# Optimization experiments

Hardware: AMD Instinct MI355X
Metric: run time of the kernel (lower is better)

Reference implementation:

```python
import jax, jax.numpy as jnp
import numpy as np

N = 100000; E = 3200000; B = 4096
F = 128; H = 128; T1 = 574; T2 = 152; MH = 128
BN_INV = float(1.0 / np.sqrt(1.0 + 1e-5))  # eval-mode BatchNorm1d, running_mean=0, running_var=1


def setup_inputs() -> dict:
    key = jax.random.key(0)
    ks = jax.random.split(key, 16)
    def w(k, shape):
        return (jax.random.normal(k, shape, jnp.float32) / np.sqrt(shape[0])).astype(jnp.float32)
    return {
        "feats": jax.random.normal(ks[0], (N, F), jnp.float32),
        "src": jax.random.randint(ks[1], (E,), 0, N, dtype=jnp.int32),
        "dst": jax.random.randint(ks[2], (E,), 0, N, dtype=jnp.int32),
        "graph_ids": jnp.sort(jax.random.randint(ks[3], (N,), 0, B, dtype=jnp.int32)),
        "W1": w(ks[4], (F, H)), "b1": jnp.zeros((H,), jnp.float32),
        "resW1": w(ks[5], (F, H)), "resb1": jnp.zeros((H,), jnp.float32),
        "W2": w(ks[6], (H, H)), "b2": jnp.zeros((H,), jnp.float32),
        "resW2": w(ks[7], (H, H)), "resb2": jnp.zeros((H,), jnp.float32),
        "aw_W": w(ks[8], (H, 1)), "aw_b": jnp.zeros((1,), jnp.float32),
        "orW1": w(ks[9], (2 * H, MH)), "orb1": jnp.zeros((MH,), jnp.float32),
        "org": jnp.ones((MH,), jnp.float32), "orbeta": jnp.zeros((MH,), jnp.float32),
        "orW2": w(ks[10], (MH, T1)), "orb2": jnp.zeros((T1,), jnp.float32),
        "scW1": w(ks[11], (2 * H + T1, MH)), "scb1": jnp.zeros((MH,), jnp.float32),
        "scg": jnp.ones((MH,), jnp.float32), "scbeta": jnp.zeros((MH,), jnp.float32),
        "scW2": w(ks[12], (MH, T2)), "scb2": jnp.zeros((T2,), jnp.float32),
    }


def _gcn_layer(feats, src, dst, W, b, resW, resb, out_norm, in_norm):
    # GraphConv with norm='both': D_out^{-1/2} on source, sum over edges, D_in^{-1/2} on dest.
    h = (feats * out_norm[:, None]) @ W                       # [N, H]
    agg = jax.ops.segment_sum(h[src], dst, num_segments=N)    # gather-compute-scatter
    out = jax.nn.relu(agg * in_norm[:, None] + b)             # activation inside GraphConv
    return out + jax.nn.relu(feats @ resW + resb)             # dgllife residual branch


def _mlp(x, Wa, ba, gam, bet, Wb, bb):
    # dgllife MLPPredictor: Dropout(0) -> Linear -> ReLU -> BatchNorm1d(eval) -> Linear
    z = jax.nn.relu(x @ Wa + ba)
    z = gam * (z * BN_INV) + bet
    return z @ Wb + bb


def _forward(feats, src, dst, graph_ids, W1, b1, resW1, resb1, W2, b2, resW2, resb2,
             aw_W, aw_b, orW1, orb1, org, orbeta, orW2, orb2,
             scW1, scb1, scg, scbeta, scW2, scb2):
    ones = jnp.ones((E,), jnp.float32)
    out_norm = jnp.clip(jax.ops.segment_sum(ones, src, num_segments=N), 1.0) ** -0.5
    in_norm = jnp.clip(jax.ops.segment_sum(ones, dst, num_segments=N), 1.0) ** -0.5
    h = _gcn_layer(feats, src, dst, W1, b1, resW1, resb1, out_norm, in_norm)
    h = _gcn_layer(h, src, dst, W2, b2, resW2, resb2, out_norm, in_norm)
    # WeightedSumAndMax readout
    aw = jax.nn.sigmoid(h @ aw_W + aw_b)                      # [N, 1] atom weights
    hsum = jax.ops.segment_sum(aw * h, graph_ids, num_segments=B)
    hmax = jax.ops.segment_max(h, graph_ids, num_segments=B)
    hmax = jnp.where(jnp.isfinite(hmax), hmax, 0.0)           # guard empty graphs
    g = jnp.concatenate([hsum, hmax], axis=1)                 # [B, 2H]
    or_logits = _mlp(g, orW1, orb1, org, orbeta, orW2, orb2)  # [B, T1]
    scent = _mlp(jnp.concatenate([g, or_logits], axis=1), scW1, scb1, scg, scbeta, scW2, scb2)
    return or_logits, scent


def reference(feats, src, dst, graph_ids, W1, b1, resW1, resb1, W2, b2, resW2, resb2,
              aw_W, aw_b, orW1, orb1, org, orbeta, orW2, orb2,
              scW1, scb1, scg, scbeta, scW2, scb2):
    return _forward(feats, src, dst, graph_ids, W1, b1, resW1, resb1, W2, b2, resW2, resb2,
                    aw_W, aw_b, orW1, orb1, org, orbeta, orW2, orb2,
                    scW1, scb1, scg, scbeta, scW2, scb2)
```

## Files before the change

kernel.cpp:

```cpp
#include <hip/hip_runtime.h>

#define NN 100000
#define EE 3200000
#define NGRAPH 4096
#define BN_INV_F 0.99999500003749981f
#define PAD 80
#define SHIFT 8
#define NBUCK 391
#define CHUNK 8192
#define NBLK 391
#define SCAN_N (2 * NBUCK * NBLK)
#define SCHUNK 2048
#define SBLKS ((SCAN_N + SCHUNK - 1) / SCHUNK)

typedef __attribute__((ext_vector_type(8))) short short8v;
typedef __attribute__((ext_vector_type(4))) float f32x4;

__device__ inline ushort f2bf(float f) {
  uint u = __builtin_bit_cast(uint, f);
  u += 0x7fff + ((u >> 16) & 1);
  return (ushort)(u >> 16);
}
__device__ inline float bf_lo(uint v) { return __builtin_bit_cast(float, v << 16); }
__device__ inline float bf_hi(uint v) { return __builtin_bit_cast(float, v & 0xffff0000u); }

__global__ __launch_bounds__(256) void count_ab(const int* __restrict__ src,
                                                const int* __restrict__ dst,
                                                int* __restrict__ cnt) {
  __shared__ int hd[NBUCK], hs[NBUCK];
  int t = threadIdx.x, blk = blockIdx.x;
  for (int i = t; i < NBUCK; i += 256) { hd[i] = 0; hs[i] = 0; }
  __syncthreads();
  int base = blk * CHUNK;
#pragma unroll 4
  for (int j = 0; j < 32; j++) {
    int e = base + j * 256 + t;
    if (e < EE) {
      atomicAdd(&hd[((unsigned)dst[e]) >> SHIFT], 1);
      atomicAdd(&hs[((unsigned)src[e]) >> SHIFT], 1);
    }
  }
  __syncthreads();
  for (int i = t; i < NBUCK; i += 256) {
    cnt[i * NBLK + blk] = hd[i];
    cnt[(NBUCK + i) * NBLK + blk] = hs[i];
  }
}

__global__ __launch_bounds__(256) void scan1(const int* __restrict__ cnt,
                                             int* __restrict__ partial) {
  __shared__ int red[256];
  int b = blockIdx.x, t = threadIdx.x;
  int s = 0;
  for (int j = 0; j < 8; j++) { int i = b * SCHUNK + j * 256 + t; if (i < SCAN_N) s += cnt[i]; }
  red[t] = s;
  __syncthreads();
  for (int off = 128; off > 0; off >>= 1) {
    if (t < off) red[t] += red[t + off];
    __syncthreads();
  }
  if (t == 0) partial[b] = red[0];
}

__global__ void scan2(int* __restrict__ partial) {
  if (threadIdx.x == 0) {
    int run = 0;
    for (int i = 0; i < SBLKS; i++) { int v = partial[i]; partial[i] = run; run += v; }
  }
}

__global__ __launch_bounds__(256) void scan3(int* __restrict__ cnt,
                                             const int* __restrict__ partial) {
  __shared__ int wsum[4];
  int b = blockIdx.x, t = threadIdx.x;
  int lane = t & 63, wid = t >> 6;
  int base = b * SCHUNK + t * 8;
  int v[8];
#pragma unroll
  for (int j = 0; j < 8; j++) { int i = base + j; v[j] = (i < SCAN_N) ? cnt[i] : 0; }
  int s = ((v[0] + v[1]) + (v[2] + v[3])) + ((v[4] + v[5]) + (v[6] + v[7]));
  int inc = s;
#pragma unroll
  for (int off = 1; off < 64; off <<= 1) {
    int u = __shfl_up(inc, off);
    if (lane >= off) inc += u;
  }
  if (lane == 63) wsum[wid] = inc;
  __syncthreads();
  int woff = 0;
  for (int w = 0; w < wid; w++) woff += wsum[w];
  int excl = partial[b] + woff + (inc - s);
#pragma unroll
  for (int j = 0; j < 8; j++) {
    int i = base + j;
    if (i < SCAN_N) cnt[i] = excl;
    excl += v[j];
  }
}

__global__ __launch_bounds__(256) void scatter_c(const int* __restrict__ src,
                                                 const int* __restrict__ dst,
                                                 const int* __restrict__ off,
                                                 int2* __restrict__ ebuf,
                                                 int* __restrict__ sbuf) {
  __shared__ int cd[NBUCK], cs[NBUCK];
  int t = threadIdx.x, blk = blockIdx.x;
  for (int i = t; i < NBUCK; i += 256) {
    cd[i] = off[i * NBLK + blk];
    cs[i] = off[(NBUCK + i) * NBLK + blk] - EE;
  }
  __syncthreads();
  int base = blk * CHUNK;
#pragma unroll 4
  for (int j = 0; j < 32; j++) {
    int e = base + j * 256 + t;
    if (e < EE) {
      int d = dst[e], s = src[e];
      int p = atomicAdd(&cd[((unsigned)d) >> SHIFT], 1);
      ebuf[p] = make_int2(d, s);
      int q = atomicAdd(&cs[((unsigned)s) >> SHIFT], 1);
      sbuf[q] = s;
    }
  }
}

__global__ __launch_bounds__(256) void pass_dd(const int* __restrict__ off,
                                               const int2* __restrict__ ebuf,
                                               const int* __restrict__ sbuf,
                                               int* __restrict__ csrp,
                                               int* __restrict__ icnt,
                                               float* __restrict__ inrm,
                                               float* __restrict__ onrm) {
  __shared__ int cur[256], cur2[256];
  int t = threadIdx.x, b = blockIdx.x;
  cur[t] = 0; cur2[t] = 0;
  __syncthreads();
  int node0 = b << SHIFT;
  int start = off[b * NBLK];
  int end = (b == NBUCK - 1) ? EE : off[(b + 1) * NBLK];
  for (int e = start + t; e < end; e += 256) {
    int2 p = ebuf[e];
    int pos = atomicAdd(&cur[p.x - node0], 1);
    if (pos < PAD) csrp[(size_t)p.x * PAD + pos] = p.y;
  }
  int s2 = off[(NBUCK + b) * NBLK] - EE;
  int e2 = (b == NBUCK - 1) ? EE : off[(NBUCK + b + 1) * NBLK] - EE;
  for (int e = s2 + t; e < e2; e += 256)
    atomicAdd(&cur2[sbuf[e] - node0], 1);
  __syncthreads();
  int node = node0 + t;
  if (node < NN) {
    int c = cur[t];
    icnt[node] = c;
    inrm[node] = rsqrtf(fmaxf((float)c, 1.f));
    onrm[node] = rsqrtf(fmaxf((float)cur2[t], 1.f));
  }
}

__global__ __launch_bounds__(256) void conv_all(
    const float* __restrict__ W1, const float* __restrict__ rW1,
    const float* __restrict__ W2, const float* __restrict__ rW2,
    const float* __restrict__ oW1, const float* __restrict__ oW2,
    const float* __restrict__ sW1, const float* __restrict__ sW2,
    ushort* __restrict__ Wt1, ushort* __restrict__ Wr1,
    ushort* __restrict__ Wt2, ushort* __restrict__ Wr2,
    ushort* __restrict__ Wm1, ushort* __restrict__ Wm2,
    ushort* __restrict__ Wm3, ushort* __restrict__ Wm4)
{
  int b = blockIdx.x;
  const float* W; ushort* O; int K, N, Kpad, c;
  if (b < 512) {
    int which = b >> 7; c = b & 127;
    K = 128; N = 128; Kpad = 128;
    W = which == 0 ? W1 : which == 1 ? rW1 : which == 2 ? W2 : rW2;
    O = which == 0 ? Wt1 : which == 1 ? Wr1 : which == 2 ? Wt2 : Wr2;
  } else if (b < 640)  { c = b - 512;  W = oW1; O = Wm1; K = 256; N = 128; Kpad = 256; }
  else if (b < 1216)   { c = b - 640;  W = oW2; O = Wm2; K = 128; N = 574; Kpad = 128; }
  else if (b < 1344)   { c = b - 1216; W = sW1; O = Wm3; K = 830; N = 128; Kpad = 832; }
  else                 { c = b - 1344; W = sW2; O = Wm4; K = 128; N = 152; Kpad = 128; }
  for (int k = threadIdx.x; k < Kpad; k += 256)
    O[(size_t)c * Kpad + k] = (c < N && k < K) ? f2bf(W[(size_t)k * N + c]) : (ushort)0;
}

__global__ __launch_bounds__(256) void conv_x(const float* __restrict__ X,
                                              ushort* __restrict__ Xb) {
  int i = blockIdx.x * 256 + threadIdx.x;
  float4 v = *(const float4*)&X[(size_t)i * 4];
  ushort o[4] = {f2bf(v.x), f2bf(v.y), f2bf(v.z), f2bf(v.w)};
  *(ushort4*)&Xb[(size_t)i * 4] = *(ushort4*)o;
}

template<int MODE>
__global__ __launch_bounds__(256) void fused_layer(
    const ushort* __restrict__ Xg, const float* __restrict__ gscale,
    const int* __restrict__ csrp, const int* __restrict__ icnt,
    const ushort* __restrict__ Xr,
    const ushort* __restrict__ Wt, const ushort* __restrict__ Wr,
    const float* __restrict__ innorm,
    const float* __restrict__ bias, const float* __restrict__ resb,
    ushort* __restrict__ outb, float* __restrict__ outf,
    const float* __restrict__ awW, const float* __restrict__ awb,
    float* __restrict__ aw)
{
  __shared__ uint agg[64 * 68];
  int t = threadIdx.x;
  int lane = t & 63, wid = t >> 6;
  int r0 = blockIdx.x * 64;
  const uint* T32 = (const uint*)Xg;

  for (int nn = 0; nn < 16; nn++) {
    int node = r0 + wid * 16 + nn;
    float a0 = 0.f, a1 = 0.f, b0 = 0.f, b1 = 0.f;
    float c0 = 0.f, c1 = 0.f, d0 = 0.f, d1 = 0.f;
    float e0 = 0.f, e1 = 0.f, f0 = 0.f, f1 = 0.f;
    float g0 = 0.f, g1 = 0.f, h0 = 0.f, h1 = 0.f;
    if (node < NN) {
      int cnt = icnt[node]; if (cnt > PAD) cnt = PAD;
      const int* row = csrp + (size_t)node * PAD;
      int j = 0;
      for (; j + 7 < cnt; j += 8) {
        int r0i = row[j],     r1i = row[j + 1], r2i = row[j + 2], r3i = row[j + 3];
        int r4i = row[j + 4], r5i = row[j + 5], r6i = row[j + 6], r7i = row[j + 7];
        float w0 = gscale[r0i], w1 = gscale[r1i], w2 = gscale[r2i], w3 = gscale[r3i];
        float w4 = gscale[r4i], w5 = gscale[r5i], w6 = gscale[r6i], w7 = gscale[r7i];
        uint v0 = T32[(size_t)r0i * 64 + lane];
        uint v1 = T32[(size_t)r1i * 64 + lane];
        uint v2 = T32[(size_t)r2i * 64 + lane];
        uint v3 = T32[(size_t)r3i * 64 + lane];
        uint v4 = T32[(size_t)r4i * 64 + lane];
        uint v5 = T32[(size_t)r5i * 64 + lane];
        uint v6 = T32[(size_t)r6i * 64 + lane];
        uint v7 = T32[(size_t)r7i * 64 + lane];
        a0 = fmaf(w0, bf_lo(v0), a0); a1 = fmaf(w0, bf_hi(v0), a1);
        b0 = fmaf(w1, bf_lo(v1), b0); b1 = fmaf(w1, bf_hi(v1), b1);
        c0 = fmaf(w2, bf_lo(v2), c0); c1 = fmaf(w2, bf_hi(v2), c1);
        d0 = fmaf(w3, bf_lo(v3), d0); d1 = fmaf(w3, bf_hi(v3), d1);
        e0 = fmaf(w4, bf_lo(v4), e0); e1 = fmaf(w4, bf_hi(v4), e1);
        f0 = fmaf(w5, bf_lo(v5), f0); f1 = fmaf(w5, bf_hi(v5), f1);
        g0 = fmaf(w6, bf_lo(v6), g0); g1 = fmaf(w6, bf_hi(v6), g1);
        h0 = fmaf(w7, bf_lo(v7), h0); h1 = fmaf(w7, bf_hi(v7), h1);
      }
      for (; j < cnt; j++) {
        int ri = row[j];
        float w = gscale[ri];
        uint v = T32[(size_t)ri * 64 + lane];
        a0 = fmaf(w, bf_lo(v), a0); a1 = fmaf(w, bf_hi(v), a1);
      }
    }
    float s0 = ((a0 + b0) + (c0 + d0)) + ((e0 + f0) + (g0 + h0));
    float s1 = ((a1 + b1) + (c1 + d1)) + ((e1 + f1) + (g1 + h1));
    agg[(wid * 16 + nn) * 68 + lane] = (uint)f2bf(s0) | ((uint)f2bf(s1) << 16);
  }
  __syncthreads();

  int cl = lane & 15, kh = lane >> 4;
  short8v a1v[4], a2v[4];
  const uint* arow = agg + (size_t)(wid * 16 + cl) * 68;
#pragma unroll
  for (int kk = 0; kk < 4; kk++)
    a1v[kk] = *(const short8v*)(arow + kk * 16 + kh * 4);
  int xrow = r0 + wid * 16 + cl; if (xrow > NN - 1) xrow = NN - 1;
#pragma unroll
  for (int kk = 0; kk < 4; kk++)
    a2v[kk] = *(const short8v*)(Xr + (size_t)xrow * 128 + kk * 32 + kh * 8);

  f32x4 acc1[8], acc2[8];
#pragma unroll
  for (int i = 0; i < 8; i++) { acc1[i] = (f32x4){0.f,0.f,0.f,0.f}; acc2[i] = acc1[i]; }
#pragma unroll
  for (int ct = 0; ct < 8; ct++) {
#pragma unroll
    for (int kk = 0; kk < 4; kk++) {
      short8v bt = *(const short8v*)(Wt + (size_t)(ct * 16 + cl) * 128 + kk * 32 + kh * 8);
      short8v br = *(const short8v*)(Wr + (size_t)(ct * 16 + cl) * 128 + kk * 32 + kh * 8);
      acc1[ct] = __builtin_amdgcn_mfma_f32_16x16x32_bf16(a1v[kk], bt, acc1[ct], 0, 0, 0);
      acc2[ct] = __builtin_amdgcn_mfma_f32_16x16x32_bf16(a2v[kk], br, acc2[ct], 0, 0, 0);
    }
  }

#pragma unroll
  for (int r = 0; r < 4; r++) {
    int row = r0 + wid * 16 + kh * 4 + r;
    if (row >= NN) continue;
    float inr = innorm[row];
    float pr = 0.f;
#pragma unroll
    for (int ct = 0; ct < 8; ct++) {
      int col = ct * 16 + cl;
      float g  = acc1[ct][r] * inr + bias[col];
      float rs = acc2[ct][r] + resb[col];
      float v = fmaxf(g, 0.f) + fmaxf(rs, 0.f);
      if (MODE == 1) outb[(size_t)row * 128 + col] = f2bf(v);
      else { outf[(size_t)row * 128 + col] = v; pr += v * awW[col]; }
    }
    if (MODE == 2) {
#pragma unroll
      for (int off = 1; off < 16; off <<= 1) pr += __shfl_xor(pr, off);
      if (cl == 0) aw[row] = 1.f / (1.f + expf(-(pr + awb[0])));
    }
  }
}

__global__ void readout_kernel(const float* __restrict__ h,
                               const float* __restrict__ aw,
                               const int* __restrict__ gid,
                               ushort* __restrict__ xc)
{
  int gg = blockIdx.x;
  int c  = threadIdx.x;
  int lo = 0, hi = NN;
  while (lo < hi) { int mid = (lo + hi) >> 1; if (gid[mid] < gg) lo = mid + 1; else hi = mid; }
  int start = lo;
  hi = NN;
  while (lo < hi) { int mid = (lo + hi) >> 1; if (gid[mid] < gg + 1) lo = mid + 1; else hi = mid; }
  int end = lo;
  float s = 0.f, m = 0.f;
  for (int n = start; n < end; n++) {
    float v = h[(size_t)n * 128 + c];
    s += aw[n] * v;
    m = fmaxf(m, v);
  }
  xc[(size_t)gg * 256 + c]       = f2bf(s);
  xc[(size_t)gg * 256 + 128 + c] = f2bf(m);
}

__global__ __launch_bounds__(256) void head2_mfma(
    const ushort* __restrict__ xc,
    const ushort* __restrict__ Wm1, const float* __restrict__ orb1,
    const float* __restrict__ org, const float* __restrict__ orbeta,
    const ushort* __restrict__ Wm2, const float* __restrict__ orb2,
    const ushort* __restrict__ Wm3, const float* __restrict__ scb1,
    const float* __restrict__ scg, const float* __restrict__ scbeta,
    const ushort* __restrict__ Wm4, const float* __restrict__ scb2,
    float* __restrict__ out_or, float* __restrict__ out_sc)
{
  __shared__ ushort zl[16][136];
  __shared__ ushort lg[16][584];
  int lane = threadIdx.x & 63;
  int wid  = threadIdx.x >> 6;
  int r0   = blockIdx.x * 16;
  int cl = lane & 15, kh = lane >> 4;
  int arow = r0 + cl;

  {
    short8v a[8];
#pragma unroll
    for (int kk = 0; kk < 8; kk++)
      a[kk] = *(const short8v*)(xc + (size_t)arow * 256 + kk * 32 + kh * 8);
    for (int ct = wid; ct < 8; ct += 4) {
      f32x4 acc = (f32x4){0.f, 0.f, 0.f, 0.f};
#pragma unroll
      for (int kk = 0; kk < 8; kk++) {
        short8v b = *(const short8v*)(Wm1 + (size_t)(ct * 16 + cl) * 256 + kk * 32 + kh * 8);
        acc = __builtin_amdgcn_mfma_f32_16x16x32_bf16(a[kk], b, acc, 0, 0, 0);
      }
      int col = ct * 16 + cl;
      float bz = orb1[col], gm = org[col], bt = orbeta[col];
#pragma unroll
      for (int r = 0; r < 4; r++) {
        float v = acc[r] + bz;
        zl[kh * 4 + r][col] = f2bf(gm * (fmaxf(v, 0.f) * BN_INV_F) + bt);
      }
    }
  }
  __syncthreads();

  {
    short8v za[4];
#pragma unroll
    for (int kk = 0; kk < 4; kk++)
      za[kk] = *(const short8v*)&zl[cl][kk * 32 + kh * 8];
    for (int ct = wid; ct < 36; ct += 4) {
      f32x4 acc = (f32x4){0.f, 0.f, 0.f, 0.f};
#pragma unroll
      for (int kk = 0; kk < 4; kk++) {
        short8v b = *(const short8v*)(Wm2 + (size_t)(ct * 16 + cl) * 128 + kk * 32 + kh * 8);
        acc = __builtin_amdgcn_mfma_f32_16x16x32_bf16(za[kk], b, acc, 0, 0, 0);
      }
      int col = ct * 16 + cl;
      if (col < 574) {
        float bz = orb2[col];
#pragma unroll
        for (int r = 0; r < 4; r++) {
          int row = r0 + kh * 4 + r;
          float v = acc[r] + bz;
          out_or[(size_t)row * 574 + col] = v;
          lg[kh * 4 + r][col] = f2bf(v);
        }
      } else {
#pragma unroll
        for (int r = 0; r < 4; r++) lg[kh * 4 + r][col] = 0;
      }
    }
  }
  __syncthreads();

  {
    short8v a[26];
#pragma unroll
    for (int kk = 0; kk < 8; kk++)
      a[kk] = *(const short8v*)(xc + (size_t)arow * 256 + kk * 32 + kh * 8);
#pragma unroll
    for (int kk = 8; kk < 26; kk++)
      a[kk] = *(const short8v*)&lg[cl][(kk - 8) * 32 + kh * 8];
    for (int ct = wid; ct < 8; ct += 4) {
      f32x4 acc = (f32x4){0.f, 0.f, 0.f, 0.f};
#pragma unroll
      for (int kk = 0; kk < 26; kk++) {
        short8v b = *(const short8v*)(Wm3 + (size_t)(ct * 16 + cl) * 832 + kk * 32 + kh * 8);
        acc = __builtin_amdgcn_mfma_f32_16x16x32_bf16(a[kk], b, acc, 0, 0, 0);
      }
      int col = ct * 16 + cl;
      float bz = scb1[col], gm = scg[col], bt = scbeta[col];
#pragma unroll
      for (int r = 0; r < 4; r++) {
        float v = acc[r] + bz;
        zl[kh * 4 + r][col] = f2bf(gm * (fmaxf(v, 0.f) * BN_INV_F) + bt);
      }
    }
  }
  __syncthreads();

  {
    short8v za[4];
#pragma unroll
    for (int kk = 0; kk < 4; kk++)
      za[kk] = *(const short8v*)&zl[cl][kk * 32 + kh * 8];
    for (int ct = wid; ct < 10; ct += 4) {
      f32x4 acc = (f32x4){0.f, 0.f, 0.f, 0.f};
#pragma unroll
      for (int kk = 0; kk < 4; kk++) {
        short8v b = *(const short8v*)(Wm4 + (size_t)(ct * 16 + cl) * 128 + kk * 32 + kh * 8);
        acc = __builtin_amdgcn_mfma_f32_16x16x32_bf16(za[kk], b, acc, 0, 0, 0);
      }
      int col = ct * 16 + cl;
      if (col < 152) {
        float bz = scb2[col];
#pragma unroll
        for (int r = 0; r < 4; r++) {
          int row = r0 + kh * 4 + r;
          out_sc[(size_t)row * 152 + col] = acc[r] + bz;
        }
      }
    }
  }
}

extern "C" void kernel_launch(void* const* d_in, const int* in_sizes, int n_in,
                              void* d_out, int out_size, void* d_ws, size_t ws_size,
                              hipStream_t stream) {
  const float* feats  = (const float*)d_in[0];
  const int*   src    = (const int*)d_in[1];
  const int*   dst    = (const int*)d_in[2];
  const int*   gid    = (const int*)d_in[3];
  const float* W1     = (const float*)d_in[4];
  const float* b1     = (const float*)d_in[5];
  const float* resW1  = (const float*)d_in[6];
  const float* resb1  = (const float*)d_in[7];
  const float* W2     = (const float*)d_in[8];
  const float* b2     = (const float*)d_in[9];
  const float* resW2  = (const float*)d_in[10];
  const float* resb2  = (const float*)d_in[11];
  const float* awW    = (const float*)d_in[12];
  const float* awb    = (const float*)d_in[13];
  const float* orW1   = (const float*)d_in[14];
  const float* orb1   = (const float*)d_in[15];
  const float* org    = (const float*)d_in[16];
  const float* orbeta = (const float*)d_in[17];
  const float* orW2   = (const float*)d_in[18];
  const float* orb2   = (const float*)d_in[19];
  const float* scW1   = (const float*)d_in[20];
  const float* scb1   = (const float*)d_in[21];
  const float* scg    = (const float*)d_in[22];
  const float* scbeta = (const float*)d_in[23];
  const float* scW2   = (const float*)d_in[24];
  const float* scb2   = (const float*)d_in[25];

  char* base = (char*)d_ws;
  ushort* Xb = (ushort*)base;
  ushort* Lb = Xb + (size_t)NN * 128;
  float*  Hf = (float*)(Lb + (size_t)NN * 128);
  int2*   ebuf = (int2*)Hf;
  int*    sbuf = (int*)(Hf + (size_t)NN * 64);
  ushort* xc  = (ushort*)(Hf + (size_t)NN * 128);
  ushort* Wt1 = xc + (size_t)NGRAPH * 256;
  ushort* Wr1 = Wt1 + 128 * 128;
  ushort* Wt2 = Wr1 + 128 * 128;
  ushort* Wr2 = Wt2 + 128 * 128;
  ushort* Wm1 = Wr2 + 128 * 128;
  ushort* Wm2 = Wm1 + 128 * 256;
  ushort* Wm3 = Wm2 + 576 * 128;
  ushort* Wm4 = Wm3 + 128 * 832;
  float* onrm = (float*)(Wm4 + 160 * 128);
  float* inrm = onrm + NN;
  float* aw   = inrm + NN;
  int* icnt    = (int*)(aw + NN);
  int* cnt     = icnt + NN;
  int* partial = cnt + SCAN_N;
  int* csrp    = partial + SBLKS;

  float* out_or = (float*)d_out;
  float* out_sc = out_or + (size_t)NGRAPH * 574;

  count_ab<<<NBLK, 256, 0, stream>>>(src, dst, cnt);
  scan1<<<SBLKS, 256, 0, stream>>>(cnt, partial);
  scan2<<<1, 64, 0, stream>>>(partial);
  scan3<<<SBLKS, 256, 0, stream>>>(cnt, partial);
  scatter_c<<<NBLK, 256, 0, stream>>>(src, dst, cnt, ebuf, sbuf);
  pass_dd<<<NBUCK, 256, 0, stream>>>(cnt, ebuf, sbuf, csrp, icnt, inrm, onrm);
  conv_all<<<1504, 256, 0, stream>>>(W1, resW1, W2, resW2, orW1, orW2, scW1, scW2,
                                     Wt1, Wr1, Wt2, Wr2, Wm1, Wm2, Wm3, Wm4);
  conv_x<<<12500, 256, 0, stream>>>(feats, Xb);

  int grid = (NN + 63) / 64;
  fused_layer<1><<<grid, 256, 0, stream>>>(Xb, onrm, csrp, icnt, Xb, Wt1, Wr1,
                                           inrm, b1, resb1, Lb, nullptr,
                                           nullptr, nullptr, nullptr);
  fused_layer<2><<<grid, 256, 0, stream>>>(Lb, onrm, csrp, icnt, Lb, Wt2, Wr2,
                                           inrm, b2, resb2, nullptr, Hf,
                                           awW, awb, aw);
  readout_kernel<<<NGRAPH, 128, 0, stream>>>(Hf, aw, gid, xc);
  head2_mfma<<<NGRAPH / 16, 256, 0, stream>>>(xc, Wm1, orb1, org, orbeta, Wm2, orb2,
                                              Wm3, scb1, scg, scbeta, Wm4, scb2,
                                              out_or, out_sc);
}
```

Before: 660.7 us.

## Split fused gather+GEMM layer into separate gather and dual-GEMM kernels

Each fused GCN layer kernel is split in two. A standalone gather kernel handles one node per wavefront with many small blocks and writes the aggregated bf16 rows to a new global buffer. A separate dual-GEMM kernel then reads that buffer for the MFMA matmuls. The intent is better latency hiding and occupancy for the irregular gather, since it no longer runs 16 nodes serially per wave inside a large shared-memory block. The cost is an extra global write and read of a 100000x128 bf16 buffer per layer, plus two more kernel launches.

Result: faster. 581.9 us (-11.9%).

```diff
diff --git a/kernel.cpp b/kernel.cpp
--- a/kernel.cpp
+++ b/kernel.cpp
@@ -190,11 +190,59 @@
   *(ushort4*)&Xb[(size_t)i * 4] = *(ushort4*)o;
 }
 
+__global__ __launch_bounds__(256) void gather_sc(const ushort* __restrict__ Xg,
+                                                 const float* __restrict__ gscale,
+                                                 const int* __restrict__ csrp,
+                                                 const int* __restrict__ icnt,
+                                                 ushort* __restrict__ Gbo) {
+  int n  = blockIdx.x * 4 + (threadIdx.x >> 6);
+  int c2 = threadIdx.x & 63;
+  if (n >= NN) return;
+  int cnt = icnt[n]; if (cnt > PAD) cnt = PAD;
+  const int* row = csrp + (size_t)n * PAD;
+  const uint* T32 = (const uint*)Xg;
+  float a0 = 0.f, a1 = 0.f, b0 = 0.f, b1 = 0.f;
+  float c0 = 0.f, c1 = 0.f, d0 = 0.f, d1 = 0.f;
+  float e0 = 0.f, e1 = 0.f, f0 = 0.f, f1 = 0.f;
+  float g0 = 0.f, g1 = 0.f, h0 = 0.f, h1 = 0.f;
+  int j = 0;
+  for (; j + 7 < cnt; j += 8) {
+    int r0i = row[j],     r1i = row[j + 1], r2i = row[j + 2], r3i = row[j + 3];
+    int r4i = row[j + 4], r5i = row[j + 5], r6i = row[j + 6], r7i = row[j + 7];
+    float w0 = gscale[r0i], w1 = gscale[r1i], w2 = gscale[r2i], w3 = gscale[r3i];
+    float w4 = gscale[r4i], w5 = gscale[r5i], w6 = gscale[r6i], w7 = gscale[r7i];
+    uint v0 = T32[(size_t)r0i * 64 + c2];
+    uint v1 = T32[(size_t)r1i * 64 + c2];
+    uint v2 = T32[(size_t)r2i * 64 + c2];
+    uint v3 = T32[(size_t)r3i * 64 + c2];
+    uint v4 = T32[(size_t)r4i * 64 + c2];
+    uint v5 = T32[(size_t)r5i * 64 + c2];
+    uint v6 = T32[(size_t)r6i * 64 + c2];
+    uint v7 = T32[(size_t)r7i * 64 + c2];
+    a0 = fmaf(w0, bf_lo(v0), a0); a1 = fmaf(w0, bf_hi(v0), a1);
+    b0 = fmaf(w1, bf_lo(v1), b0); b1 = fmaf(w1, bf_hi(v1), b1);
+    c0 = fmaf(w2, bf_lo(v2), c0); c1 = fmaf(w2, bf_hi(v2), c1);
+    d0 = fmaf(w3, bf_lo(v3), d0); d1 = fmaf(w3, bf_hi(v3), d1);
+    e0 = fmaf(w4, bf_lo(v4), e0); e1 = fmaf(w4, bf_hi(v4), e1);
+    f0 = fmaf(w5, bf_lo(v5), f0); f1 = fmaf(w5, bf_hi(v5), f1);
+    g0 = fmaf(w6, bf_lo(v6), g0); g1 = fmaf(w6, bf_hi(v6), g1);
+    h0 = fmaf(w7, bf_lo(v7), h0); h1 = fmaf(w7, bf_hi(v7), h1);
+  }
+  for (; j < cnt; j++) {
+    int ri = row[j];
+    float w = gscale[ri];
+    uint v = T32[(size_t)ri * 64 + c2];
+    a0 = fmaf(w, bf_lo(v), a0); a1 = fmaf(w, bf_hi(v), a1);
+  }
+  float s0 = ((a0 + b0) + (c0 + d0)) + ((e0 + f0) + (g0 + h0));
+  float s1 = ((a1 + b1) + (c1 + d1)) + ((e1 + f1) + (g1 + h1));
+  uint o = (uint)f2bf(s0) | ((uint)f2bf(s1) << 16);
+  ((uint*)Gbo)[(size_t)n * 64 + c2] = o;
+}
+
 template<int MODE>
-__global__ __launch_bounds__(256) void fused_layer(
-    const ushort* __restrict__ Xg, const float* __restrict__ gscale,
-    const int* __restrict__ csrp, const int* __restrict__ icnt,
-    const ushort* __restrict__ Xr,
+__global__ __launch_bounds__(256) void dual_gemm(
+    const ushort* __restrict__ Gb, const ushort* __restrict__ Xr,
     const ushort* __restrict__ Wt, const ushort* __restrict__ Wr,
     const float* __restrict__ innorm,
     const float* __restrict__ bias, const float* __restrict__ resb,
@@ -202,67 +250,18 @@
     const float* __restrict__ awW, const float* __restrict__ awb,
     float* __restrict__ aw)
 {
-  __shared__ uint agg[64 * 68];
-  int t = threadIdx.x;
-  int lane = t & 63, wid = t >> 6;
-  int r0 = blockIdx.x * 64;
-  const uint* T32 = (const uint*)Xg;
-
-  for (int nn = 0; nn < 16; nn++) {
-    int node = r0 + wid * 16 + nn;
-    float a0 = 0.f, a1 = 0.f, b0 = 0.f, b1 = 0.f;
-    float c0 = 0.f, c1 = 0.f, d0 = 0.f, d1 = 0.f;
-    float e0 = 0.f, e1 = 0.f, f0 = 0.f, f1 = 0.f;
-    float g0 = 0.f, g1 = 0.f, h0 = 0.f, h1 = 0.f;
-    if (node < NN) {
-      int cnt = icnt[node]; if (cnt > PAD) cnt = PAD;
-      const int* row = csrp + (size_t)node * PAD;
-      int j = 0;
-      for (; j + 7 < cnt; j += 8) {
-        int r0i = row[j],     r1i = row[j + 1], r2i = row[j + 2], r3i = row[j + 3];
-        int r4i = row[j + 4], r5i = row[j + 5], r6i = row[j + 6], r7i = row[j + 7];
-        float w0 = gscale[r0i], w1 = gscale[r1i], w2 = gscale[r2i], w3 = gscale[r3i];
-        float w4 = gscale[r4i], w5 = gscale[r5i], w6 = gscale[r6i], w7 = gscale[r7i];
-        uint v0 = T32[(size_t)r0i * 64 + lane];
-        uint v1 = T32[(size_t)r1i * 64 + lane];
-        uint v2 = T32[(size_t)r2i * 64 + lane];
-        uint v3 = T32[(size_t)r3i * 64 + lane];
-        uint v4 = T32[(size_t)r4i * 64 + lane];
-        uint v5 = T32[(size_t)r5i * 64 + lane];
-        uint v6 = T32[(size_t)r6i * 64 + lane];
-        uint v7 = T32[(size_t)r7i * 64 + lane];
-        a0 = fmaf(w0, bf_lo(v0), a0); a1 = fmaf(w0, bf_hi(v0), a1);
-        b0 = fmaf(w1, bf_lo(v1), b0); b1 = fmaf(w1, bf_hi(v1), b1);
-        c0 = fmaf(w2, bf_lo(v2), c0); c1 = fmaf(w2, bf_hi(v2), c1);
-        d0 = fmaf(w3, bf_lo(v3), d0); d1 = fmaf(w3, bf_hi(v3), d1);
-        e0 = fmaf(w4, bf_lo(v4), e0); e1 = fmaf(w4, bf_hi(v4), e1);
-        f0 = fmaf(w5, bf_lo(v5), f0); f1 = fmaf(w5, bf_hi(v5), f1);
-        g0 = fmaf(w6, bf_lo(v6), g0); g1 = fmaf(w6, bf_hi(v6), g1);
-        h0 = fmaf(w7, bf_lo(v7), h0); h1 = fmaf(w7, bf_hi(v7), h1);
-      }
-      for (; j < cnt; j++) {
-        int ri = row[j];
-        float w = gscale[ri];
-        uint v = T32[(size_t)ri * 64 + lane];
-        a0 = fmaf(w, bf_lo(v), a0); a1 = fmaf(w, bf_hi(v), a1);
-      }
-    }
-    float s0 = ((a0 + b0) + (c0 + d0)) + ((e0 + f0) + (g0 + h0));
-    float s1 = ((a1 + b1) + (c1 + d1)) + ((e1 + f1) + (g1 + h1));
-    agg[(wid * 16 + nn) * 68 + lane] = (uint)f2bf(s0) | ((uint)f2bf(s1) << 16);
-  }
-  __syncthreads();
-
+  int lane = threadIdx.x & 63;
+  int wid  = threadIdx.x >> 6;
+  int r0   = blockIdx.x * 64 + wid * 16;
   int cl = lane & 15, kh = lane >> 4;
+
+  int arow = r0 + cl; if (arow > NN - 1) arow = NN - 1;
   short8v a1v[4], a2v[4];
-  const uint* arow = agg + (size_t)(wid * 16 + cl) * 68;
-#pragma unroll
-  for (int kk = 0; kk < 4; kk++)
-    a1v[kk] = *(const short8v*)(arow + kk * 16 + kh * 4);
-  int xrow = r0 + wid * 16 + cl; if (xrow > NN - 1) xrow = NN - 1;
-#pragma unroll
-  for (int kk = 0; kk < 4; kk++)
-    a2v[kk] = *(const short8v*)(Xr + (size_t)xrow * 128 + kk * 32 + kh * 8);
+#pragma unroll
+  for (int kk = 0; kk < 4; kk++) {
+    a1v[kk] = *(const short8v*)(Gb + (size_t)arow * 128 + kk * 32 + kh * 8);
+    a2v[kk] = *(const short8v*)(Xr + (size_t)arow * 128 + kk * 32 + kh * 8);
+  }
 
   f32x4 acc1[8], acc2[8];
 #pragma unroll
@@ -280,7 +279,7 @@
 
 #pragma unroll
   for (int r = 0; r < 4; r++) {
-    int row = r0 + wid * 16 + kh * 4 + r;
+    int row = r0 + kh * 4 + r;
     if (row >= NN) continue;
     float inr = innorm[row];
     float pr = 0.f;
@@ -479,7 +478,8 @@
   char* base = (char*)d_ws;
   ushort* Xb = (ushort*)base;
   ushort* Lb = Xb + (size_t)NN * 128;
-  float*  Hf = (float*)(Lb + (size_t)NN * 128);
+  ushort* Gb = Lb + (size_t)NN * 128;
+  float*  Hf = (float*)(Gb + (size_t)NN * 128);
   int2*   ebuf = (int2*)Hf;
   int*    sbuf = (int*)(Hf + (size_t)NN * 64);
   ushort* xc  = (ushort*)(Hf + (size_t)NN * 128);
@@ -512,13 +512,14 @@
                                      Wt1, Wr1, Wt2, Wr2, Wm1, Wm2, Wm3, Wm4);
   conv_x<<<12500, 256, 0, stream>>>(feats, Xb);
 
-  int grid = (NN + 63) / 64;
-  fused_layer<1><<<grid, 256, 0, stream>>>(Xb, onrm, csrp, icnt, Xb, Wt1, Wr1,
-                                           inrm, b1, resb1, Lb, nullptr,
-                                           nullptr, nullptr, nullptr);
-  fused_layer<2><<<grid, 256, 0, stream>>>(Lb, onrm, csrp, icnt, Lb, Wt2, Wr2,
-                                           inrm, b2, resb2, nullptr, Hf,
-                                           awW, awb, aw);
+  int ggrid = (NN + 3) / 4;
+  int dgrid = (NN + 63) / 64;
+  gather_sc<<<ggrid, 256, 0, stream>>>(Xb, onrm, csrp, icnt, Gb);
+  dual_gemm<1><<<dgrid, 256, 0, stream>>>(Gb, Xb, Wt1, Wr1, inrm, b1, resb1,
+                                          Lb, nullptr, nullptr, nullptr, nullptr);
+  gather_sc<<<ggrid, 256, 0, stream>>>(Lb, onrm, csrp, icnt, Gb);
+  dual_gemm<2><<<dgrid, 256, 0, stream>>>(Gb, Lb, Wt2, Wr2, inrm, b2, resb2,
+                                          nullptr, Hf, awW, awb, aw);
   readout_kernel<<<NGRAPH, 128, 0, stream>>>(Hf, aw, gid, xc);
   head2_mfma<<<NGRAPH / 16, 256, 0, stream>>>(xc, Wm1, orb1, org, orbeta, Wm2, orb2,
                                               Wm3, scb1, scg, scbeta, Wm4, scb2,
```
